# Optimization experiments

Hardware: AMD Instinct MI355X
Metric: run time of the kernel (lower is better)

The kernel has to match this reference:

```python
import jax, jax.numpy as jnp
import numpy as np

BUCKET_SIZE = 64
N_HASHES = 8
SELF_MASK_VAL = -1e5
EPS = 1e-6


def look_one_back(x):
    # concat each block with the previous block (wrap-around), along block-inner axis
    prev = jnp.roll(x, 1, axis=1)
    return jnp.concatenate([x, prev], axis=2)


def setup_inputs() -> dict:
    key = jax.random.key(0)
    k1, k2, k3 = jax.random.split(key, 3)
    B, S, D = 8, 4096, 64
    n_buckets = S // BUCKET_SIZE  # 64
    qk = jax.random.normal(k1, (B, S, D), dtype=jnp.float32)
    v = jax.random.normal(k2, (B, S, D), dtype=jnp.float32)
    rotations = jax.random.normal(k3, (1, D, N_HASHES, n_buckets // 2), dtype=jnp.float32)
    return {"qk": qk, "v": v, "rotations": rotations}


def reference(qk, v, rotations):
    B, S, D = qk.shape
    n_buckets = S // BUCKET_SIZE
    n_bins = n_buckets

    # --- hash_vectors ---
    rot = jnp.broadcast_to(rotations, (B, D, N_HASHES, n_buckets // 2))
    rotated = jnp.einsum('btf,bfhi->bhti', qk, rot)            # [B,H,S,nb/2]
    rotated = jnp.concatenate([rotated, -rotated], axis=-1)    # [B,H,S,nb]
    buckets = jnp.argmax(rotated, axis=-1)                     # [B,H,S]
    offsets = (jnp.arange(N_HASHES) * n_buckets)[None, :, None]
    buckets = (buckets + offsets).reshape(B, N_HASHES * S)     # [B,H*S]

    # --- sort tokens by (bucket, position) ---
    ticker = jnp.arange(N_HASHES * S)[None, :]
    buckets_and_t = S * buckets + (ticker % S)
    sticker = jnp.argsort(buckets_and_t, axis=-1)              # stable sort
    undo_sort = jnp.argsort(sticker, axis=-1)
    st = sticker % S                                           # original positions

    sqk = jnp.take_along_axis(qk, st[..., None], axis=1)       # [B,H*S,D]
    sv = jnp.take_along_axis(v, st[..., None], axis=1)

    n_blocks = N_HASHES * n_bins
    bq_t = st.reshape(B, n_blocks, -1)                         # [B,nb,bs]
    bqk = sqk.reshape(B, n_blocks, -1, D)
    bv = sv.reshape(B, n_blocks, -1, D)

    bq = bqk
    # make_unit_length
    bk = bqk * jax.lax.rsqrt(jnp.sum(bqk * bqk, axis=-1, keepdims=True) + EPS)
    bk = look_one_back(bk)                                     # [B,nb,2bs,D]
    bv = look_one_back(bv)
    bkv_t = look_one_back(bq_t[..., None])[..., 0]             # [B,nb,2bs]

    dots = jnp.einsum('bhie,bhje->bhij', bq, bk) * (D ** -0.5)  # [B,nb,bs,2bs]

    # self-mask (as written in source: keep dots where positions equal, -1e5 elsewhere)
    self_mask = bq_t[:, :, :, None] == bkv_t[:, :, None, :]
    dots = jnp.where(self_mask, dots, SELF_MASK_VAL)

    dots_lse = jax.scipy.special.logsumexp(dots, axis=-1, keepdims=True)
    probs = jnp.exp(dots - dots_lse)
    bo = jnp.einsum('buij,buje->buie', probs, bv)              # [B,nb,bs,D]

    so = bo.reshape(B, N_HASHES * S, D)
    slogits = dots_lse.reshape(B, N_HASHES * S)

    # unsort
    o = jnp.take_along_axis(so, undo_sort[..., None], axis=1)
    logits = jnp.take_along_axis(slogits, undo_sort, axis=1)

    # combine over hash rounds
    o = o.reshape(B, N_HASHES, S, D)
    logits = logits.reshape(B, N_HASHES, S, 1)
    w = jnp.exp(logits - jax.scipy.special.logsumexp(logits, axis=1, keepdims=True))
    out = jnp.sum(o * w, axis=1)                               # [B,S,D]
    return out, buckets
```

## Files before the change

kernel.cpp:

```cpp
#include <hip/hip_runtime.h>

#define BB 8
#define SS 4096
#define DD 64
#define NH 8
#define NBKT 64
#define OUT_V_ELEMS (BB*SS*DD)

__global__ __launch_bounds__(128, 2) void lsh_hash_kernel(
    const float* __restrict__ qk,
    const float* __restrict__ v,
    const float* __restrict__ rot,
    float* __restrict__ out)
{
    __shared__ float q_s[128 * 64];
    __shared__ float rot_s[64 * 128];

    const int tid = threadIdx.x;
    const int blk = blockIdx.x;
    const int b   = blk >> 6;
    const int hq  = (blk >> 5) & 1;
    const int ch  = blk & 31;
    const int t0  = ch * 128;

    {
        const float4* v4 = (const float4*)v;
        float4*       o4 = (float4*)out;
        const int base = blk * 1024 + tid;
#pragma unroll
        for (int j = 0; j < 8; ++j)
            o4[base + j * 128] = v4[base + j * 128];
    }

    {
        const float4* qg = (const float4*)qk;
#pragma unroll
        for (int k = 0; k < 16; ++k) {
            const int p   = k * 128 + tid;
            const int tok = p >> 4, fc = p & 15;
            const float4 x = qg[(b * SS + t0 + tok) * 16 + fc];
            *(float4*)&q_s[tok * 64 + ((fc ^ ((tok >> 3) & 7)) << 2)] = x;
        }
    }
    {
        const float4* rg = (const float4*)rot;
#pragma unroll
        for (int k = 0; k < 16; ++k) {
            const int p = k * 128 + tid;
            const int f = p >> 5, c = p & 31;
            const float4 x = rg[f * 64 + hq * 32 + c];
            const int slot = (c & 3) * 8 + (c >> 2);
            *(float4*)&rot_s[f * 128 + slot * 4] = x;
        }
    }
    __syncthreads();

    const int lane = tid & 63;
    const int wv   = tid >> 6;
    const int tx   = lane & 7;
    const int ty   = lane >> 3;
    const int trow = (wv * 64 + tx * 8) * 64;
    const int rbase = ty * 4;

    float acc[8][16];
#pragma unroll
    for (int a = 0; a < 8; ++a)
#pragma unroll
        for (int c = 0; c < 16; ++c) acc[a][c] = 0.0f;

    float4 qA[8], qB[8];
    float4 rP[4], rQ[4];

#define LOADQ(dst, fq_)                                                    \
    {                                                                      \
        const int qc = (((fq_) ^ tx) << 2);                                \
        _Pragma("unroll")                                                  \
        for (int a = 0; a < 8; ++a)                                        \
            dst[a] = *(const float4*)&q_s[trow + a * 64 + qc];             \
    }
#define LOADR(dst, f_)                                                     \
    {                                                                      \
        const int ff = ((f_) < 64 ? (f_) : 0);                             \
        _Pragma("unroll")                                                  \
        for (int p = 0; p < 4; ++p)                                        \
            dst[p] = *(const float4*)&rot_s[ff * 128 + p * 32 + rbase];    \
    }
#define FMAS(qr, CMP, R)                                                   \
    {                                                                      \
        const float rr[16] = {R[0].x, R[0].y, R[0].z, R[0].w,              \
                              R[1].x, R[1].y, R[1].z, R[1].w,              \
                              R[2].x, R[2].y, R[2].z, R[2].w,              \
                              R[3].x, R[3].y, R[3].z, R[3].w};             \
        _Pragma("unroll")                                                  \
        for (int a = 0; a < 8; ++a) {                                      \
            const float qf = qr[a].CMP;                                    \
            _Pragma("unroll")                                              \
            for (int c = 0; c < 16; ++c)                                   \
                acc[a][c] = fmaf(qf, rr[c], acc[a][c]);                    \
        }                                                                  \
    }

    LOADQ(qA, 0);
    LOADR(rP, 0);
#pragma unroll 1
    for (int fq = 0; fq < 16; fq += 2) {
        const int f0 = fq * 4;
        LOADQ(qB, fq + 1);
        LOADR(rQ, f0 + 1); FMAS(qA, x, rP);
        LOADR(rP, f0 + 2); FMAS(qA, y, rQ);
        LOADR(rQ, f0 + 3); FMAS(qA, z, rP);
        LOADR(rP, f0 + 4); FMAS(qA, w, rQ);
        if (fq + 2 < 16) LOADQ(qA, fq + 2);
        LOADR(rQ, f0 + 5); FMAS(qB, x, rP);
        LOADR(rP, f0 + 6); FMAS(qB, y, rQ);
        LOADR(rQ, f0 + 7); FMAS(qB, z, rP);
        LOADR(rP, f0 + 8); FMAS(qB, w, rQ);
    }

    const int h     = hq * 4 + (ty >> 1);
    const int dbase = (ty & 1) * 16;
    float* bout = out + OUT_V_ELEMS + b * (NH * SS) + h * SS + t0 + wv * 64 + tx * 8;

#pragma unroll
    for (int a = 0; a < 8; ++a) {
        float pv = acc[a][0]; int pi = dbase;
        float nv = -acc[a][0]; int ni = dbase;
#pragma unroll
        for (int c = 1; c < 16; ++c) {
            const float x = acc[a][c];
            if (x  > pv) { pv = x;  pi = dbase + c; }
            if (-x > nv) { nv = -x; ni = dbase + c; }
        }
        const float opv = __shfl_xor(pv, 8);
        const int   opi = __shfl_xor(pi, 8);
        const float onv = __shfl_xor(nv, 8);
        const int   oni = __shfl_xor(ni, 8);
        if (opv > pv || (opv == pv && opi < pi)) { pv = opv; pi = opi; }
        if (onv > nv || (onv == nv && oni < ni)) { nv = onv; ni = oni; }
        const int idx = (pv >= nv) ? pi : (ni + 32);
        if ((ty & 1) == 0) bout[a] = (float)(idx + h * NBKT);
    }
#undef LOADQ
#undef LOADR
#undef FMAS
}

extern "C" void kernel_launch(void* const* d_in, const int* in_sizes, int n_in,
                              void* d_out, int out_size, void* d_ws, size_t ws_size,
                              hipStream_t stream) {
    const float* qk  = (const float*)d_in[0];
    const float* v   = (const float*)d_in[1];
    const float* rot = (const float*)d_in[2];
    float* out = (float*)d_out;
    hipLaunchKernelGGL(lsh_hash_kernel, dim3(512), dim3(128), 0, stream,
                       qk, v, rot, out);
}
```

Before: 25.73 us.

## Remap hash GEMM to 256 threads with 8x8 per-thread tiles

```diff
diff --git a/kernel.cpp b/kernel.cpp
--- a/kernel.cpp
+++ b/kernel.cpp
@@ -7,7 +7,7 @@
 #define NBKT 64
 #define OUT_V_ELEMS (BB*SS*DD)
 
-__global__ __launch_bounds__(128, 2) void lsh_hash_kernel(
+__global__ __launch_bounds__(256, 2) void lsh_hash_kernel(
     const float* __restrict__ qk,
     const float* __restrict__ v,
     const float* __restrict__ rot,
@@ -28,15 +28,15 @@
         float4*       o4 = (float4*)out;
         const int base = blk * 1024 + tid;
 #pragma unroll
-        for (int j = 0; j < 8; ++j)
-            o4[base + j * 128] = v4[base + j * 128];
+        for (int j = 0; j < 4; ++j)
+            o4[base + j * 256] = v4[base + j * 256];
     }
 
     {
         const float4* qg = (const float4*)qk;
 #pragma unroll
-        for (int k = 0; k < 16; ++k) {
-            const int p   = k * 128 + tid;
+        for (int k = 0; k < 8; ++k) {
+            const int p   = k * 256 + tid;
             const int tok = p >> 4, fc = p & 15;
             const float4 x = qg[(b * SS + t0 + tok) * 16 + fc];
             *(float4*)&q_s[tok * 64 + ((fc ^ ((tok >> 3) & 7)) << 2)] = x;
@@ -45,35 +45,32 @@
     {
         const float4* rg = (const float4*)rot;
 #pragma unroll
-        for (int k = 0; k < 16; ++k) {
-            const int p = k * 128 + tid;
+        for (int k = 0; k < 8; ++k) {
+            const int p = k * 256 + tid;
             const int f = p >> 5, c = p & 31;
             const float4 x = rg[f * 64 + hq * 32 + c];
-            const int slot = (c & 3) * 8 + (c >> 2);
-            *(float4*)&rot_s[f * 128 + slot * 4] = x;
+            *(float4*)&rot_s[f * 128 + c * 4] = x;
         }
     }
     __syncthreads();
 
-    const int lane = tid & 63;
-    const int wv   = tid >> 6;
-    const int tx   = lane & 7;
-    const int ty   = lane >> 3;
-    const int trow = (wv * 64 + tx * 8) * 64;
-    const int rbase = ty * 4;
+    const int tx    = tid & 15;
+    const int ty    = tid >> 4;
+    const int trow  = tx * 8 * 64;
+    const int rbase = ty * 8;
 
-    float acc[8][16];
+    float acc[8][8];
 #pragma unroll
     for (int a = 0; a < 8; ++a)
 #pragma unroll
-        for (int c = 0; c < 16; ++c) acc[a][c] = 0.0f;
+        for (int c = 0; c < 8; ++c) acc[a][c] = 0.0f;
 
     float4 qA[8], qB[8];
-    float4 rP[4], rQ[4];
+    float4 rP[2], rQ[2];
 
 #define LOADQ(dst, fq_)                                                    \
     {                                                                      \
-        const int qc = (((fq_) ^ tx) << 2);                                \
+        const int qc = (((fq_) ^ (tx & 7)) << 2);                          \
         _Pragma("unroll")                                                  \
         for (int a = 0; a < 8; ++a)                                        \
             dst[a] = *(const float4*)&q_s[trow + a * 64 + qc];             \
@@ -81,21 +78,18 @@
 #define LOADR(dst, f_)                                                     \
     {                                                                      \
         const int ff = ((f_) < 64 ? (f_) : 0);                             \
-        _Pragma("unroll")                                                  \
-        for (int p = 0; p < 4; ++p)                                        \
-            dst[p] = *(const float4*)&rot_s[ff * 128 + p * 32 + rbase];    \
+        dst[0] = *(const float4*)&rot_s[ff * 128 + rbase];                 \
+        dst[1] = *(const float4*)&rot_s[ff * 128 + rbase + 4];             \
     }
 #define FMAS(qr, CMP, R)                                                   \
     {                                                                      \
-        const float rr[16] = {R[0].x, R[0].y, R[0].z, R[0].w,              \
-                              R[1].x, R[1].y, R[1].z, R[1].w,              \
-                              R[2].x, R[2].y, R[2].z, R[2].w,              \
-                              R[3].x, R[3].y, R[3].z, R[3].w};             \
+        const float rr[8] = {R[0].x, R[0].y, R[0].z, R[0].w,               \
+                             R[1].x, R[1].y, R[1].z, R[1].w};              \
         _Pragma("unroll")                                                  \
         for (int a = 0; a < 8; ++a) {                                      \
             const float qf = qr[a].CMP;                                    \
             _Pragma("unroll")                                              \
-            for (int c = 0; c < 16; ++c)                                   \
+            for (int c = 0; c < 8; ++c)                                    \
                 acc[a][c] = fmaf(qf, rr[c], acc[a][c]);                    \
         }                                                                  \
     }
@@ -117,28 +111,31 @@
         LOADR(rP, f0 + 8); FMAS(qB, w, rQ);
     }
 
-    const int h     = hq * 4 + (ty >> 1);
-    const int dbase = (ty & 1) * 16;
-    float* bout = out + OUT_V_ELEMS + b * (NH * SS) + h * SS + t0 + wv * 64 + tx * 8;
+    const int h     = hq * 4 + (ty >> 2);
+    const int dbase = (ty & 3) * 8;
+    float* bout = out + OUT_V_ELEMS + b * (NH * SS) + h * SS + t0 + tx * 8;
 
 #pragma unroll
     for (int a = 0; a < 8; ++a) {
         float pv = acc[a][0]; int pi = dbase;
         float nv = -acc[a][0]; int ni = dbase;
 #pragma unroll
-        for (int c = 1; c < 16; ++c) {
+        for (int c = 1; c < 8; ++c) {
             const float x = acc[a][c];
             if (x  > pv) { pv = x;  pi = dbase + c; }
             if (-x > nv) { nv = -x; ni = dbase + c; }
         }
-        const float opv = __shfl_xor(pv, 8);
-        const int   opi = __shfl_xor(pi, 8);
-        const float onv = __shfl_xor(nv, 8);
-        const int   oni = __shfl_xor(ni, 8);
-        if (opv > pv || (opv == pv && opi < pi)) { pv = opv; pi = opi; }
-        if (onv > nv || (onv == nv && oni < ni)) { nv = onv; ni = oni; }
+#pragma unroll
+        for (int m = 16; m <= 32; m <<= 1) {
+            const float opv = __shfl_xor(pv, m);
+            const int   opi = __shfl_xor(pi, m);
+            const float onv = __shfl_xor(nv, m);
+            const int   oni = __shfl_xor(ni, m);
+            if (opv > pv || (opv == pv && opi < pi)) { pv = opv; pi = opi; }
+            if (onv > nv || (onv == nv && oni < ni)) { nv = onv; ni = oni; }
+        }
         const int idx = (pv >= nv) ? pi : (ni + 32);
-        if ((ty & 1) == 0) bout[a] = (float)(idx + h * NBKT);
+        if ((ty & 3) == 0) bout[a] = (float)(idx + h * NBKT);
     }
 #undef LOADQ
 #undef LOADR
@@ -152,6 +149,6 @@
     const float* v   = (const float*)d_in[1];
     const float* rot = (const float*)d_in[2];
     float* out = (float*)d_out;
-    hipLaunchKernelGGL(lsh_hash_kernel, dim3(512), dim3(128), 0, stream,
+    hipLaunchKernelGGL(lsh_hash_kernel, dim3(512), dim3(256), 0, stream,
                        qk, v, rot, out);
 }
```

Result: faster. 24.59 us (-4.4%).
